# Optimization experiments

Measured on AMD Instinct MI355X. Metric: run time of the kernel, lower is better.

## Reference

```python
import jax, jax.numpy as jnp
import numpy as np
import math

PHI = (1.0 + math.sqrt(5.0)) / 2.0
LUT_SIZE = 4096
TWO_PI = 2.0 * math.pi


def _lut_tables():
    # 4096-entry sin/cos lookup tables over [0, 2*pi)
    grid = jnp.arange(LUT_SIZE, dtype=jnp.float32) * (TWO_PI / LUT_SIZE)
    return jnp.sin(grid), jnp.cos(grid)


def _lookup_sin_cos(theta, sin_t, cos_t):
    # nearest-entry LUT lookup: index = round(theta / (2*pi) * N) mod N
    idx = jnp.mod(jnp.round(theta * (LUT_SIZE / TWO_PI)), LUT_SIZE).astype(jnp.int32)
    return sin_t[idx], cos_t[idx]


def setup_inputs() -> dict:
    key = jax.random.key(0)
    ks = jax.random.split(key, 6)
    B, D, H = 16, 2048, 2048
    return {
        "current_state_real": jax.random.normal(ks[0], (B, D), jnp.float32),
        "current_state_imag": jax.random.normal(ks[1], (B, D), jnp.float32),
        "history_real": jax.random.normal(ks[2], (B, H, D), jnp.float32),
        "history_imag": jax.random.normal(ks[3], (B, H, D), jnp.float32),
        "ema_state": jax.random.normal(ks[4], (B, 2 * D), jnp.float32),
        "w_q": jax.random.normal(ks[5], (D,), jnp.float32) * 0.02,
        "b_q": jnp.zeros((D,), jnp.float32),
        "alpha": jnp.asarray(0.1, jnp.float32),
        "t": jnp.asarray(3.0, jnp.float32),
    }


def reference(current_state_real, current_state_imag, history_real, history_imag,
              ema_state, w_q, b_q, alpha, t):
    D = current_state_real.shape[-1]
    scale = math.sqrt(2.0 * D)
    sin_t, cos_t = _lut_tables()

    wl_q = 1.0 + jnp.abs(w_q)                      # (D,)
    t_phi = t * PHI
    theta_real = current_state_real / wl_q + b_q + t_phi   # (B, D)
    theta_imag = current_state_imag / wl_q + b_q + t_phi   # (B, D)
    _, cos_q_real = _lookup_sin_cos(theta_real, sin_t, cos_t)
    _, cos_q_imag = _lookup_sin_cos(theta_imag, sin_t, cos_t)

    # keys == values == stacked history (no projection): (B, H, 2D)
    keys = jnp.concatenate([history_real, history_imag], axis=-1)
    query_for_match = jnp.concatenate([cos_q_real, cos_q_imag], axis=-1)  # (B, 2D)

    scores = jnp.einsum('bd,bhd->bh', query_for_match, keys) / scale      # (B, H)
    weights = jax.nn.softmax(scores, axis=-1)
    retrieved = jnp.einsum('bh,bhd->bd', weights, keys)                   # (B, 2D)

    a = jax.nn.sigmoid(alpha)
    new_ema = a * retrieved + (1.0 - a) * ema_state
    return new_ema
```

## Files before the change

kernel.cpp:

```cpp
#include <hip/hip_runtime.h>
#include <math.h>

#ifndef M_PI
#define M_PI 3.14159265358979323846
#endif

#define LUT_N 4096
#define WPB 4
#define TROWS 4

__device__ __forceinline__ float lut_cos(float theta) {
    const float IDX_SCALE = (float)((double)LUT_N / (2.0 * M_PI));
    const float STEP = (float)((2.0 * M_PI) / (double)LUT_N);
    float x = theta * IDX_SCALE;
    int i = (int)rintf(x);
    i &= (LUT_N - 1);
    return cosf((float)i * STEP);
}

__global__ void qgen_kernel(const float* __restrict__ cur_r,
                            const float* __restrict__ cur_i,
                            const float* __restrict__ w_q,
                            const float* __restrict__ b_q,
                            const float* __restrict__ t_ptr,
                            float* __restrict__ q_out,
                            int B, int D) {
    int idx = blockIdx.x * blockDim.x + threadIdx.x;
    int twoD = 2 * D;
    if (idx >= B * twoD) return;
    int b = idx / twoD;
    int c = idx - b * twoD;
    int col = (c < D) ? c : c - D;
    const float* src = (c < D) ? cur_r : cur_i;
    float v = src[(size_t)b * D + col];
    float t_phi = t_ptr[0] * 1.61803398874989484820f;
    float wl = 1.0f + fabsf(w_q[col]);
    float theta = v / wl + b_q[col] + t_phi;
    q_out[idx] = lut_cos(theta);
}

typedef const __attribute__((address_space(1))) unsigned int guint;
typedef __attribute__((address_space(3))) unsigned int suint;

__device__ __forceinline__ void stage_row(const float* __restrict__ hr_row,
                                          const float* __restrict__ hi_row,
                                          float* lds_row, int lane) {
#pragma unroll
    for (int c = 0; c < 8; ++c)
        __builtin_amdgcn_global_load_lds(
            (guint*)(const void*)(hr_row + c * 256 + lane * 4),
            (suint*)(void*)(lds_row + c * 256), 16, 0, 0);
#pragma unroll
    for (int c = 0; c < 8; ++c)
        __builtin_amdgcn_global_load_lds(
            (guint*)(const void*)(hi_row + c * 256 + lane * 4),
            (suint*)(void*)(lds_row + 2048 + c * 256), 16, 0, 0);
}

__global__ __launch_bounds__(256, 1) void flash_kernel(
    const float* __restrict__ hist_r,
    const float* __restrict__ hist_i,
    const float* __restrict__ q_ws,
    float* __restrict__ r_ws,
    float* __restrict__ ml_ws,
    int H, int S) {
    const int t = threadIdx.x;
    const int lane = t & 63;
    const int wv = t >> 6;
    const int b = blockIdx.x / S;
    const int s = blockIdx.x - b * S;
    const int rows_blk = H / S;
    const int NT = rows_blk / TROWS;

    __shared__ float buf[2][TROWS][4096];
    __shared__ float sm[WPB], sl[WPB];

    const size_t row0 = (size_t)b * H + (size_t)s * rows_blk + wv;
    const float* hr_w = hist_r + row0 * 2048;
    const float* hi_w = hist_i + row0 * 2048;

    const float4* q4 = (const float4*)q_ws + (size_t)b * 1024;
    float4 qv[16];
#pragma unroll
    for (int j = 0; j < 16; ++j) qv[j] = q4[j * 64 + lane];

    float4 rv[16];
#pragma unroll
    for (int j = 0; j < 16; ++j) rv[j] = make_float4(0.f, 0.f, 0.f, 0.f);
    float m0 = -INFINITY, l = 0.f;
    const float inv_scale = 1.0f / 64.0f;

    stage_row(hr_w, hi_w, &buf[0][wv][0], lane);
    __syncthreads();

    for (int kt = 0; kt < NT; ++kt) {
        if (kt + 1 < NT)
            stage_row(hr_w + (size_t)(kt + 1) * TROWS * 2048,
                      hi_w + (size_t)(kt + 1) * TROWS * 2048,
                      &buf[(kt + 1) & 1][wv][0], lane);

        const float4* krow = (const float4*)&buf[kt & 1][wv][0];
        float4 kv[16];
#pragma unroll
        for (int j = 0; j < 16; ++j) kv[j] = krow[j * 64 + lane];

        float p = 0.f;
#pragma unroll
        for (int j = 0; j < 16; ++j)
            p += qv[j].x * kv[j].x + qv[j].y * kv[j].y +
                 qv[j].z * kv[j].z + qv[j].w * kv[j].w;
#pragma unroll
        for (int off = 32; off; off >>= 1) p += __shfl_xor(p, off);
        float sc = p * inv_scale;

        float d = sc - m0;
        float w;
        if (d > 8.0f) {
            float corr = __expf(-d);
            l *= corr;
#pragma unroll
            for (int j = 0; j < 16; ++j) {
                rv[j].x *= corr; rv[j].y *= corr;
                rv[j].z *= corr; rv[j].w *= corr;
            }
            m0 = sc;
            w = 1.0f;
        } else {
            w = __expf(d);
        }
        l += w;
#pragma unroll
        for (int j = 0; j < 16; ++j) {
            rv[j].x = fmaf(w, kv[j].x, rv[j].x);
            rv[j].y = fmaf(w, kv[j].y, rv[j].y);
            rv[j].z = fmaf(w, kv[j].z, rv[j].z);
            rv[j].w = fmaf(w, kv[j].w, rv[j].w);
        }

        __syncthreads();
    }

    if (lane == 0) { sm[wv] = m0; sl[wv] = l; }
    __syncthreads();
    float M = fmaxf(fmaxf(sm[0], sm[1]), fmaxf(sm[2], sm[3]));
    float Lb = sl[0] * __expf(sm[0] - M) + sl[1] * __expf(sm[1] - M) +
               sl[2] * __expf(sm[2] - M) + sl[3] * __expf(sm[3] - M);
    float scale = __expf(m0 - M);

    float4* sred = (float4*)&buf[0][0][0];
    for (int w = 0; w < WPB; ++w) {
        if (wv == w) {
#pragma unroll
            for (int j = 0; j < 16; ++j) {
                int idx = j * 64 + lane;
                float4 v = (w == 0) ? make_float4(0.f, 0.f, 0.f, 0.f) : sred[idx];
                v.x = fmaf(scale, rv[j].x, v.x);
                v.y = fmaf(scale, rv[j].y, v.y);
                v.z = fmaf(scale, rv[j].z, v.z);
                v.w = fmaf(scale, rv[j].w, v.w);
                sred[idx] = v;
            }
        }
        __syncthreads();
    }

    float4* ro = (float4*)r_ws + (size_t)blockIdx.x * 1024;
#pragma unroll
    for (int k = 0; k < 4; ++k) ro[t + 256 * k] = sred[t + 256 * k];
    if (t == 0) {
        ml_ws[2 * (size_t)blockIdx.x] = M;
        ml_ws[2 * (size_t)blockIdx.x + 1] = Lb;
    }
}

__global__ void combine_kernel(const float* __restrict__ r_ws,
                               const float* __restrict__ ml_ws,
                               const float* __restrict__ ema,
                               const float* __restrict__ alpha_ptr,
                               float* __restrict__ out,
                               int D, int S) {
    const int twoD = 2 * D;
    const int nc = twoD / 256;
    const int b = blockIdx.x / nc;
    const int cb = blockIdx.x - b * nc;
    const int c = cb * 256 + threadIdx.x;

    const float* ml = ml_ws + (size_t)b * S * 2;
    float M = -INFINITY;
    for (int s = 0; s < S; ++s) M = fmaxf(M, ml[2 * s]);
    float L = 0.f;
    for (int s = 0; s < S; ++s) L += ml[2 * s + 1] * __expf(ml[2 * s] - M);

    float acc = 0.f;
    const float* rb = r_ws + (size_t)b * S * twoD + c;
    for (int s = 0; s < S; ++s)
        acc = fmaf(__expf(ml[2 * s] - M), rb[(size_t)s * twoD], acc);

    float a = 1.0f / (1.0f + __expf(-alpha_ptr[0]));
    float retrieved = acc / L;
    size_t o = (size_t)b * twoD + c;
    out[o] = a * retrieved + (1.0f - a) * ema[o];
}

extern "C" void kernel_launch(void* const* d_in, const int* in_sizes, int n_in,
                              void* d_out, int out_size, void* d_ws, size_t ws_size,
                              hipStream_t stream) {
    const float* cur_r  = (const float*)d_in[0];
    const float* cur_i  = (const float*)d_in[1];
    const float* hist_r = (const float*)d_in[2];
    const float* hist_i = (const float*)d_in[3];
    const float* ema    = (const float*)d_in[4];
    const float* w_q    = (const float*)d_in[5];
    const float* b_q    = (const float*)d_in[6];
    const float* alpha  = (const float*)d_in[7];
    const float* t      = (const float*)d_in[8];

    const int D = in_sizes[5];
    const int B = in_sizes[0] / D;
    const int H = in_sizes[2] / (B * D);
    const int twoD = 2 * D;

    float* q_ws = (float*)d_ws;
    size_t q_elems = (size_t)B * twoD;

    int S = 32;
    while (S > 1) {
        size_t need = (q_elems + (size_t)B * S * twoD + (size_t)B * S * 2) * sizeof(float);
        if (need <= ws_size) break;
        S >>= 1;
    }
    float* r_ws = q_ws + q_elems;
    float* ml_ws = r_ws + (size_t)B * S * twoD;

    int qblocks = (B * twoD + 255) / 256;
    qgen_kernel<<<qblocks, 256, 0, stream>>>(cur_r, cur_i, w_q, b_q, t, q_ws, B, D);
    flash_kernel<<<B * S, 256, 0, stream>>>(hist_r, hist_i, q_ws, r_ws, ml_ws, H, S);
    combine_kernel<<<B * (twoD / 256), 256, 0, stream>>>(r_ws, ml_ws, ema, alpha,
                                                         (float*)d_out, D, S);
}
```

Measured before the change: 129.6 us.

## Decouple waves with per-wave triple-buffered LDS rings and drop block barriers

Each wave now owns a private 3-deep LDS ring and streams strided history rows on its own schedule. Explicit vmcnt waits replace the per-iteration __syncthreads, and the in-block cross-wave reduction is dropped: each wave writes its own partial (m, l, r) straight to the workspace. The grid becomes 256 blocks of 3 waves, 16 per batch. This aims to keep more loads in flight and remove barrier stalls, at the cost of more partials for the combine kernel to read and 144KB of LDS per block.

```diff
diff --git a/kernel.cpp b/kernel.cpp
--- a/kernel.cpp
+++ b/kernel.cpp
@@ -6,8 +6,8 @@
 #endif
 
 #define LUT_N 4096
-#define WPB 4
-#define TROWS 4
+#define WVS 3
+#define DEPTH 3
 
 __device__ __forceinline__ float lut_cos(float theta) {
     const float IDX_SCALE = (float)((double)LUT_N / (2.0 * M_PI));
@@ -57,58 +57,71 @@
             (suint*)(void*)(lds_row + 2048 + c * 256), 16, 0, 0);
 }
 
-__global__ __launch_bounds__(256, 1) void flash_kernel(
+__global__ __launch_bounds__(192, 1) void flash_kernel(
     const float* __restrict__ hist_r,
     const float* __restrict__ hist_i,
     const float* __restrict__ q_ws,
     float* __restrict__ r_ws,
     float* __restrict__ ml_ws,
-    int H, int S) {
+    int H, int Wb, int bpb) {
     const int t = threadIdx.x;
     const int lane = t & 63;
     const int wv = t >> 6;
-    const int b = blockIdx.x / S;
-    const int s = blockIdx.x - b * S;
-    const int rows_blk = H / S;
-    const int NT = rows_blk / TROWS;
-
-    __shared__ float buf[2][TROWS][4096];
-    __shared__ float sm[WPB], sl[WPB];
-
-    const size_t row0 = (size_t)b * H + (size_t)s * rows_blk + wv;
-    const float* hr_w = hist_r + row0 * 2048;
-    const float* hi_w = hist_i + row0 * 2048;
+    const int b = blockIdx.x / bpb;
+    const int j = (blockIdx.x - b * bpb) * WVS + wv;
+
+    __shared__ float ring[WVS][DEPTH][4096];
 
     const float4* q4 = (const float4*)q_ws + (size_t)b * 1024;
     float4 qv[16];
 #pragma unroll
-    for (int j = 0; j < 16; ++j) qv[j] = q4[j * 64 + lane];
+    for (int k = 0; k < 16; ++k) qv[k] = q4[k * 64 + lane];
+    asm volatile("s_waitcnt vmcnt(0)" ::: "memory");
+
+    const int n = (H - j + Wb - 1) / Wb;
+    const float* hr = hist_r + ((size_t)b * H + j) * 2048;
+    const float* hi = hist_i + ((size_t)b * H + j) * 2048;
+    float* myring = &ring[wv][0][0];
 
     float4 rv[16];
 #pragma unroll
-    for (int j = 0; j < 16; ++j) rv[j] = make_float4(0.f, 0.f, 0.f, 0.f);
+    for (int k = 0; k < 16; ++k) rv[k] = make_float4(0.f, 0.f, 0.f, 0.f);
     float m0 = -INFINITY, l = 0.f;
     const float inv_scale = 1.0f / 64.0f;
 
-    stage_row(hr_w, hi_w, &buf[0][wv][0], lane);
-    __syncthreads();
-
-    for (int kt = 0; kt < NT; ++kt) {
-        if (kt + 1 < NT)
-            stage_row(hr_w + (size_t)(kt + 1) * TROWS * 2048,
-                      hi_w + (size_t)(kt + 1) * TROWS * 2048,
-                      &buf[(kt + 1) & 1][wv][0], lane);
-
-        const float4* krow = (const float4*)&buf[kt & 1][wv][0];
+    for (int i = 0; i < DEPTH - 1 && i < n; ++i)
+        stage_row(hr + (size_t)i * Wb * 2048, hi + (size_t)i * Wb * 2048,
+                  myring + (i % DEPTH) * 4096, lane);
+
+    for (int i = 0; i < n; ++i) {
+        if (i + DEPTH - 1 < n) {
+            const size_t g = (size_t)(i + DEPTH - 1) * Wb * 2048;
+            stage_row(hr + g, hi + g, myring + ((i + DEPTH - 1) % DEPTH) * 4096, lane);
+        }
+        const int ahead = n - 1 - i;
+        if (ahead >= 2)      asm volatile("s_waitcnt vmcnt(32)" ::: "memory");
+        else if (ahead == 1) asm volatile("s_waitcnt vmcnt(16)" ::: "memory");
+        else                 asm volatile("s_waitcnt vmcnt(0)"  ::: "memory");
+        __builtin_amdgcn_sched_barrier(0);
+
+        const float4* krow = (const float4*)(myring + (i % DEPTH) * 4096);
         float4 kv[16];
 #pragma unroll
-        for (int j = 0; j < 16; ++j) kv[j] = krow[j * 64 + lane];
-
-        float p = 0.f;
-#pragma unroll
-        for (int j = 0; j < 16; ++j)
-            p += qv[j].x * kv[j].x + qv[j].y * kv[j].y +
-                 qv[j].z * kv[j].z + qv[j].w * kv[j].w;
+        for (int k = 0; k < 16; ++k) kv[k] = krow[k * 64 + lane];
+
+        float p0 = 0.f, p1 = 0.f, p2 = 0.f, p3 = 0.f;
+#pragma unroll
+        for (int k = 0; k < 4; ++k) {
+            p0 += qv[4*k+0].x * kv[4*k+0].x + qv[4*k+0].y * kv[4*k+0].y +
+                  qv[4*k+0].z * kv[4*k+0].z + qv[4*k+0].w * kv[4*k+0].w;
+            p1 += qv[4*k+1].x * kv[4*k+1].x + qv[4*k+1].y * kv[4*k+1].y +
+                  qv[4*k+1].z * kv[4*k+1].z + qv[4*k+1].w * kv[4*k+1].w;
+            p2 += qv[4*k+2].x * kv[4*k+2].x + qv[4*k+2].y * kv[4*k+2].y +
+                  qv[4*k+2].z * kv[4*k+2].z + qv[4*k+2].w * kv[4*k+2].w;
+            p3 += qv[4*k+3].x * kv[4*k+3].x + qv[4*k+3].y * kv[4*k+3].y +
+                  qv[4*k+3].z * kv[4*k+3].z + qv[4*k+3].w * kv[4*k+3].w;
+        }
+        float p = (p0 + p1) + (p2 + p3);
 #pragma unroll
         for (int off = 32; off; off >>= 1) p += __shfl_xor(p, off);
         float sc = p * inv_scale;
@@ -119,9 +132,9 @@
             float corr = __expf(-d);
             l *= corr;
 #pragma unroll
-            for (int j = 0; j < 16; ++j) {
-                rv[j].x *= corr; rv[j].y *= corr;
-                rv[j].z *= corr; rv[j].w *= corr;
+            for (int k = 0; k < 16; ++k) {
+                rv[k].x *= corr; rv[k].y *= corr;
+                rv[k].z *= corr; rv[k].w *= corr;
             }
             m0 = sc;
             w = 1.0f;
@@ -130,46 +143,21 @@
         }
         l += w;
 #pragma unroll
-        for (int j = 0; j < 16; ++j) {
-            rv[j].x = fmaf(w, kv[j].x, rv[j].x);
-            rv[j].y = fmaf(w, kv[j].y, rv[j].y);
-            rv[j].z = fmaf(w, kv[j].z, rv[j].z);
-            rv[j].w = fmaf(w, kv[j].w, rv[j].w);
-        }
-
-        __syncthreads();
+        for (int k = 0; k < 16; ++k) {
+            rv[k].x = fmaf(w, kv[k].x, rv[k].x);
+            rv[k].y = fmaf(w, kv[k].y, rv[k].y);
+            rv[k].z = fmaf(w, kv[k].z, rv[k].z);
+            rv[k].w = fmaf(w, kv[k].w, rv[k].w);
+        }
     }
 
-    if (lane == 0) { sm[wv] = m0; sl[wv] = l; }
-    __syncthreads();
-    float M = fmaxf(fmaxf(sm[0], sm[1]), fmaxf(sm[2], sm[3]));
-    float Lb = sl[0] * __expf(sm[0] - M) + sl[1] * __expf(sm[1] - M) +
-               sl[2] * __expf(sm[2] - M) + sl[3] * __expf(sm[3] - M);
-    float scale = __expf(m0 - M);
-
-    float4* sred = (float4*)&buf[0][0][0];
-    for (int w = 0; w < WPB; ++w) {
-        if (wv == w) {
-#pragma unroll
-            for (int j = 0; j < 16; ++j) {
-                int idx = j * 64 + lane;
-                float4 v = (w == 0) ? make_float4(0.f, 0.f, 0.f, 0.f) : sred[idx];
-                v.x = fmaf(scale, rv[j].x, v.x);
-                v.y = fmaf(scale, rv[j].y, v.y);
-                v.z = fmaf(scale, rv[j].z, v.z);
-                v.w = fmaf(scale, rv[j].w, v.w);
-                sred[idx] = v;
-            }
-        }
-        __syncthreads();
-    }
-
-    float4* ro = (float4*)r_ws + (size_t)blockIdx.x * 1024;
-#pragma unroll
-    for (int k = 0; k < 4; ++k) ro[t + 256 * k] = sred[t + 256 * k];
-    if (t == 0) {
-        ml_ws[2 * (size_t)blockIdx.x] = M;
-        ml_ws[2 * (size_t)blockIdx.x + 1] = Lb;
+    const size_t pidx = (size_t)b * Wb + j;
+    float4* ro = (float4*)r_ws + pidx * 1024;
+#pragma unroll
+    for (int k = 0; k < 16; ++k) ro[k * 64 + lane] = rv[k];
+    if (lane == 0) {
+        ml_ws[pidx * 2] = m0;
+        ml_ws[pidx * 2 + 1] = l;
     }
 }
 
@@ -223,18 +211,21 @@
     float* q_ws = (float*)d_ws;
     size_t q_elems = (size_t)B * twoD;
 
-    int S = 32;
-    while (S > 1) {
-        size_t need = (q_elems + (size_t)B * S * twoD + (size_t)B * S * 2) * sizeof(float);
+    int bpb = 256 / B; if (bpb < 1) bpb = 1;
+    while (bpb > 1) {
+        int Wb = bpb * WVS;
+        size_t need = (q_elems + (size_t)B * Wb * twoD + (size_t)B * Wb * 2) * sizeof(float);
         if (need <= ws_size) break;
-        S >>= 1;
+        bpb >>= 1;
     }
+    const int Wb = bpb * WVS;
     float* r_ws = q_ws + q_elems;
-    float* ml_ws = r_ws + (size_t)B * S * twoD;
+    float* ml_ws = r_ws + (size_t)B * Wb * twoD;
 
     int qblocks = (B * twoD + 255) / 256;
     qgen_kernel<<<qblocks, 256, 0, stream>>>(cur_r, cur_i, w_q, b_q, t, q_ws, B, D);
-    flash_kernel<<<B * S, 256, 0, stream>>>(hist_r, hist_i, q_ws, r_ws, ml_ws, H, S);
+    flash_kernel<<<B * bpb, WVS * 64, 0, stream>>>(hist_r, hist_i, q_ws, r_ws, ml_ws,
+                                                   H, Wb, bpb);
     combine_kernel<<<B * (twoD / 256), 256, 0, stream>>>(r_ws, ml_ws, ema, alpha,
-                                                         (float*)d_out, D, S);
-}
+                                                         (float*)d_out, D, Wb);
+}
```

Result: faster. 125.7 us (-3.0%).
